# Kernel optimization log

Measured on AMD Instinct MI355X. Metric: run time of the kernel, lower is better.

The kernel has to match this reference:

```python
import jax, jax.numpy as jnp
import numpy as np
from jax.scipy.special import logsumexp

B, T, V, E, H, L = 64, 256, 50000, 256, 256, 9


def setup_inputs() -> dict:
    key = jax.random.key(0)
    ks = jax.random.split(key, 10)
    lengths = jax.random.randint(ks[0], (B,), T // 2, T + 1)
    pm = jnp.arange(T)[None, :] < lengths[:, None]  # valid-token mask, padding at tail
    inp = jnp.where(pm, jax.random.randint(ks[1], (B, T), 1, V), 0).astype(jnp.int32)
    tags = jnp.where(pm, jax.random.randint(ks[2], (B, T), 0, L), 0).astype(jnp.int32)
    s = 0.05
    emb = jax.random.normal(ks[3], (V, E)) * s
    Wf = jax.random.normal(ks[4], (E, 4 * H)) * s
    Uf = jax.random.normal(ks[5], (H, 4 * H)) * s
    bf = jnp.zeros((4 * H,))
    Wb = jax.random.normal(ks[6], (E, 4 * H)) * s
    Ub = jax.random.normal(ks[7], (H, 4 * H)) * s
    bb = jnp.zeros((4 * H,))
    Wd = jax.random.normal(ks[8], (2 * H, L)) * s
    bd = jnp.zeros((L,))
    trans = jax.random.uniform(ks[9], (L, L))
    return dict(inp=inp, tags=tags, emb=emb, Wf=Wf, Uf=Uf, bf=bf,
                Wb=Wb, Ub=Ub, bb=bb, Wd=Wd, bd=bd, trans=trans)


def _lstm(x, mask, W, U, b):
    """Keras-style LSTM with masking (state + output carried through masked steps).
    x: [B,T,E], mask: [B,T] bool -> [B,T,H]."""
    h0 = jnp.zeros((x.shape[0], H), x.dtype)
    c0 = h0

    def step(carry, xm):
        h, c = carry
        xt, mt = xm
        z = xt @ W + h @ U + b  # [B,4H], gate order i,f,g,o (Keras)
        i, f, g, o = jnp.split(z, 4, axis=-1)
        c_new = jax.nn.sigmoid(f) * c + jax.nn.sigmoid(i) * jnp.tanh(g)
        h_new = jax.nn.sigmoid(o) * jnp.tanh(c_new)
        m = mt[:, None]
        h = jnp.where(m, h_new, h)
        c = jnp.where(m, c_new, c)
        return (h, c), h

    _, hs = jax.lax.scan(step, (h0, c0), (x.transpose(1, 0, 2), mask.T))
    return hs.transpose(1, 0, 2)


def _crf_log_likelihood(pot, tags, seq_lens, trans):
    """tfa.text.crf_log_likelihood: sequence_score - log_norm. pot: [B,T,L]."""
    Bv, Tv, Lv = pot.shape
    tmask = (jnp.arange(Tv)[None, :] < seq_lens[:, None]).astype(pot.dtype)
    unary = jnp.sum(jnp.take_along_axis(pot, tags[..., None], axis=-1)[..., 0] * tmask, axis=1)
    pmask = (jnp.arange(Tv - 1)[None, :] < (seq_lens - 1)[:, None]).astype(pot.dtype)
    binary = jnp.sum(trans[tags[:, :-1], tags[:, 1:]] * pmask, axis=1)

    # forward algorithm; alpha frozen once t >= seq_len (tfa uses dynamic_rnn semantics)
    def step(carry, pot_t):
        alpha, t = carry
        new = pot_t + logsumexp(alpha[:, :, None] + trans[None], axis=1)  # [B,L]
        alpha = jnp.where((t < seq_lens)[:, None], new, alpha)
        return (alpha, t + 1), None

    (alpha, _), _ = jax.lax.scan(step, (pot[:, 0, :], jnp.int32(1)),
                                 pot[:, 1:].transpose(1, 0, 2))
    log_norm = logsumexp(alpha, axis=-1)
    return unary + binary - log_norm


def reference(inp, tags, emb, Wf, Uf, bf, Wb, Ub, bb, Wd, bd, trans):
    mask = inp != 0
    seq_lens = jnp.sum(mask.astype(jnp.int32), axis=-1)
    x = jnp.take(emb, inp, axis=0)  # [B,T,E]; dropout is identity (inference)
    hf = _lstm(x, mask, Wf, Uf, bf)
    hb = _lstm(x[:, ::-1], mask[:, ::-1], Wb, Ub, bb)[:, ::-1]
    pot = jnp.concatenate([hf, hb], axis=-1) @ Wd + bd  # [B,T,L]
    ll = _crf_log_likelihood(pot, tags, seq_lens, trans)
    loss = -jnp.mean(ll / seq_lens.astype(pot.dtype))
    return pot, seq_lens, loss
```

## Files before the change

### kernel.cpp

```cpp
#include <hip/hip_runtime.h>

#define B_ 64
#define T_ 256
#define E_ 256
#define H_ 256
#define G4 1024
#define L_ 9

typedef __attribute__((ext_vector_type(8))) short bf16x8;
typedef __attribute__((ext_vector_type(4))) float f32x4;
typedef __attribute__((ext_vector_type(4))) unsigned uint4v;
typedef _Float16 half2v __attribute__((ext_vector_type(2)));

__device__ __forceinline__ ushort f2bf(float x){
  unsigned u = __float_as_uint(x);
  unsigned r = (u + 0x7FFFu + ((u >> 16) & 1u)) >> 16;
  return (ushort)r;
}
__device__ __forceinline__ float bf2f(unsigned u16v){
  return __uint_as_float(u16v << 16);
}
__device__ __forceinline__ float fsig(float x){
  return __builtin_amdgcn_rcpf(1.f + __expf(-x));
}
__device__ __forceinline__ float ftanh(float x){
  return 1.f - 2.f * __builtin_amdgcn_rcpf(__expf(2.f * x) + 1.f);
}
__device__ __forceinline__ int sdot4(unsigned a, unsigned b, int c){
#if __has_builtin(__builtin_amdgcn_sdot4)
  return __builtin_amdgcn_sdot4((int)a, (int)b, c, false);
#else
  int r = c;
  #pragma unroll
  for (int j = 0; j < 4; j++){
    int av = (int)(signed char)((a >> (8 * j)) & 0xFF);
    int bv = (int)(signed char)((b >> (8 * j)) & 0xFF);
    r += av * bv;
  }
  return r;
#endif
}

__global__ void k_prep(const int* __restrict__ inp, const float* __restrict__ emb,
                       const float* __restrict__ Wf, const float* __restrict__ Wb,
                       const float* __restrict__ Uf, const float* __restrict__ Ub,
                       ushort* __restrict__ WT, unsigned* __restrict__ Uq,
                       float* __restrict__ su, ushort* __restrict__ X,
                       int* __restrict__ lens, float* __restrict__ out_len){
  int bid = blockIdx.x, tid = threadIdx.x;
  if (bid < 2048){
    int idx = bid * 256 + tid;
    int dir = idx >> 18; int rem = idx & 262143;
    int n = rem >> 8, k = rem & 255;
    const float* W = dir ? Wb : Wf;
    WT[idx] = f2bf(W[k * G4 + n]);
  } else if (bid < 4096){
    int idx = bid - 2048;
    int dir = idx >> 10, cc = idx & 1023;
    int u = cc & 255, g = cc >> 8;
    const float* U = dir ? Ub : Uf;
    float v = U[tid * G4 + cc];
    __shared__ float red[4];
    __shared__ float ssu;
    __shared__ char qb[256];
    float a = fabsf(v);
    #pragma unroll
    for (int off = 32; off; off >>= 1) a = fmaxf(a, __shfl_xor(a, off));
    int lane = tid & 63, w = tid >> 6;
    if (lane == 0) red[w] = a;
    __syncthreads();
    if (tid == 0){
      float m = fmaxf(fmaxf(red[0], red[1]), fmaxf(red[2], red[3]));
      float s = fmaxf(m, 1e-20f) * (1.f / 127.f);
      ssu = s;
      su[idx] = s;
    }
    __syncthreads();
    float s = ssu;
    int q = __float2int_rn(v / s);
    q = max(-127, min(127, q));
    qb[tid] = (char)q;
    __syncthreads();
    if (tid < 64){
      int khalf = tid >> 5, kk = tid & 31;
      Uq[dir * 65536 + u * 256 + khalf * 128 + g * 32 + kk] =
          *(const unsigned*)&qb[tid * 4];
    }
  } else if (bid < 6144){
    int idx = (bid - 4096) * 256 + tid;
    int m = idx >> 5, koff = (idx & 31) * 8;
    int tok = inp[m];
    const float* src = emb + (size_t)tok * E_ + koff;
    float4 a = *(const float4*)src;
    float4 b = *(const float4*)(src + 4);
    uint4 o;
    o.x = (unsigned)f2bf(a.x) | ((unsigned)f2bf(a.y) << 16);
    o.y = (unsigned)f2bf(a.z) | ((unsigned)f2bf(a.w) << 16);
    o.z = (unsigned)f2bf(b.x) | ((unsigned)f2bf(b.y) << 16);
    o.w = (unsigned)f2bf(b.z) | ((unsigned)f2bf(b.w) << 16);
    *(uint4*)(X + m * E_ + koff) = o;
  } else {
    int w = tid >> 6, lane = tid & 63;
    int b = (bid - 6144) * 4 + w;
    int c = 0;
    for (int t = lane; t < T_; t += 64) c += (inp[b * T_ + t] != 0);
    for (int off = 32; off; off >>= 1) c += __shfl_xor(c, off);
    if (lane == 0){ lens[b] = c; out_len[b] = (float)c; }
  }
}

__global__ __launch_bounds__(256) void k_gemm(const ushort* __restrict__ X,
        const ushort* __restrict__ WT, const float* __restrict__ bf_,
        const float* __restrict__ bb_, ushort* __restrict__ Zpf, ushort* __restrict__ Zpb){
  int zi = blockIdx.z;
  const ushort* wt = WT + zi * 262144;
  const float* bias = zi ? bb_ : bf_;
  ushort* Zp = zi ? Zpb : Zpf;
  int m0 = blockIdx.x * 128, n0 = blockIdx.y * 128;
  __shared__ ushort As[128][40];
  __shared__ ushort Bs[128][40];
  int tid = threadIdx.x;
  int sr = tid >> 1, sk = (tid & 1) * 16;
  const ushort* xg = X + (m0 + sr) * E_ + sk;
  const ushort* wg = wt + (n0 + sr) * E_ + sk;
  f32x4 acc[4][4] = {};
  int lane = tid & 63, wv = tid >> 6;
  int wr = wv >> 1, wc = wv & 1;
  int lrow = lane & 15, kf = (lane >> 4) * 8;
  for (int k0 = 0; k0 < E_; k0 += 32){
    uint4 a0 = *(const uint4*)(xg + k0);
    uint4 a1 = *(const uint4*)(xg + k0 + 8);
    uint4 b0 = *(const uint4*)(wg + k0);
    uint4 b1 = *(const uint4*)(wg + k0 + 8);
    *(uint4*)&As[sr][sk]     = a0;  *(uint4*)&As[sr][sk + 8] = a1;
    *(uint4*)&Bs[sr][sk]     = b0;  *(uint4*)&Bs[sr][sk + 8] = b1;
    __syncthreads();
    bf16x8 af[4], bfr[4];
    #pragma unroll
    for (int i = 0; i < 4; i++) af[i]  = *(const bf16x8*)&As[wr * 64 + i * 16 + lrow][kf];
    #pragma unroll
    for (int i = 0; i < 4; i++) bfr[i] = *(const bf16x8*)&Bs[wc * 64 + i * 16 + lrow][kf];
    #pragma unroll
    for (int i = 0; i < 4; i++)
      #pragma unroll
      for (int j = 0; j < 4; j++)
        acc[i][j] = __builtin_amdgcn_mfma_f32_16x16x32_bf16(af[i], bfr[j], acc[i][j], 0, 0, 0);
    __syncthreads();
  }
  int crow = (lane >> 4) * 4;
  #pragma unroll
  for (int j = 0; j < 4; j++){
    int col = n0 + wc * 64 + j * 16 + lrow;
    float bv = bias[col];
    int gg = col >> 8, jj = col & 255;
    #pragma unroll
    for (int i = 0; i < 4; i++){
      int rbase = m0 + wr * 64 + i * 16 + crow;
      #pragma unroll
      for (int r = 0; r < 4; r++)
        Zp[((size_t)(rbase + r) * 256 + jj) * 4 + gg] = f2bf(acc[i][j][r] + bv);
    }
  }
}

__global__ __launch_bounds__(512, 1) void k_recur11(
    const ushort* __restrict__ Zpf, const ushort* __restrict__ Zpb,
    const unsigned* __restrict__ Uq, const float* __restrict__ su,
    const int* __restrict__ lens, ushort* __restrict__ hf16, ushort* __restrict__ hb16){
  int bid = blockIdx.x;
  int dir = bid >> 6, b = bid & 63;
  const uint2* Zp = (const uint2*)(dir ? Zpb : Zpf);
  ushort* H = dir ? hb16 : hf16;
  int tid = threadIdx.x;
  int u = tid >> 1, khalf = tid & 1;
  float sc0 = su[dir * 1024 +        u] * (1.f / 127.f);
  float sc1 = su[dir * 1024 + 256 +  u] * (1.f / 127.f);
  float sc2 = su[dir * 1024 + 512 +  u] * (1.f / 127.f);
  float sc3 = su[dir * 1024 + 768 +  u] * (1.f / 127.f);
  int alen = lens[b];

  uint4v uq[4][8];
  {
    const unsigned* p = Uq + dir * 65536 + u * 256 + khalf * 128;
    #pragma unroll
    for (int g = 0; g < 4; g++)
      #pragma unroll
      for (int i = 0; i < 8; i++)
        asm volatile("global_load_dwordx4 %0, %1, off"
                     : "=v"(uq[g][i]) : "v"(p + g * 32 + i * 4));
    asm volatile("s_waitcnt vmcnt(0)" ::: "memory");
    __builtin_amdgcn_sched_barrier(0);
  }

  __shared__ unsigned hq[2][64];
  if (tid < 128) ((unsigned*)hq)[tid] = 0u;
  __syncthreads();

  float c_st = 0.f, h_st = 0.f;
  int t0 = dir ? 255 : 0;
  uint2 zw = Zp[(size_t)(b * 256 + t0) * 256 + u];

  for (int s_ = 0; s_ < 256; ++s_){
    int t = dir ? (255 - s_) : s_;
    int tn = dir ? (t - 1) : (t + 1);
    int cur = s_ & 1, nxt = cur ^ 1;
    uint2 zw_n = uint2{0u, 0u};
    if (s_ < 255) zw_n = Zp[(size_t)(b * 256 + tn) * 256 + u];
    int a0 = 0, a1 = 0, a2 = 0, a3 = 0;
    const uint4* hp = (const uint4*)&hq[cur][khalf * 32];
    #pragma unroll
    for (int i = 0; i < 8; i++){
      uint4 hv = hp[i];
      a0 = sdot4(uq[0][i][0], hv.x, a0);  a0 = sdot4(uq[0][i][1], hv.y, a0);
      a0 = sdot4(uq[0][i][2], hv.z, a0);  a0 = sdot4(uq[0][i][3], hv.w, a0);
      a1 = sdot4(uq[1][i][0], hv.x, a1);  a1 = sdot4(uq[1][i][1], hv.y, a1);
      a1 = sdot4(uq[1][i][2], hv.z, a1);  a1 = sdot4(uq[1][i][3], hv.w, a1);
      a2 = sdot4(uq[2][i][0], hv.x, a2);  a2 = sdot4(uq[2][i][1], hv.y, a2);
      a2 = sdot4(uq[2][i][2], hv.z, a2);  a2 = sdot4(uq[2][i][3], hv.w, a2);
      a3 = sdot4(uq[3][i][0], hv.x, a3);  a3 = sdot4(uq[3][i][1], hv.y, a3);
      a3 = sdot4(uq[3][i][2], hv.z, a3);  a3 = sdot4(uq[3][i][3], hv.w, a3);
    }
    a0 += __shfl_xor(a0, 1);
    a1 += __shfl_xor(a1, 1);
    a2 += __shfl_xor(a2, 1);
    a3 += __shfl_xor(a3, 1);
    float zi = bf2f(zw.x & 0xffffu) + (float)a0 * sc0;
    float zf = bf2f(zw.x >> 16)     + (float)a1 * sc1;
    float zg = bf2f(zw.y & 0xffffu) + (float)a2 * sc2;
    float zo = bf2f(zw.y >> 16)     + (float)a3 * sc3;
    if (t < alen){
      c_st = fsig(zf) * c_st + fsig(zi) * ftanh(zg);
      h_st = fsig(zo) * ftanh(c_st);
    }
    if (khalf == 0){
      int ri = __float2int_rn(h_st * 127.f);
      ((char*)hq[nxt])[u] = (char)ri;
      H[(size_t)(b * 256 + t) * H_ + u] = f2bf(h_st);
    }
    __syncthreads();
    zw = zw_n;
  }
}

__global__ __launch_bounds__(256) void k_pot(const ushort* __restrict__ hf16,
        const ushort* __restrict__ hb16, const float* __restrict__ Wd,
        const float* __restrict__ bd, float* __restrict__ out, int* __restrict__ cnt){
  if (blockIdx.x == 0 && threadIdx.x == 0) *cnt = 0;
  int lane = threadIdx.x & 63, wid = threadIdx.x >> 6;
  int m = blockIdx.x * 4 + wid;
  uint2 ua = *(const uint2*)&hf16[(size_t)m * H_ + lane * 4];
  uint2 ub = *(const uint2*)&hb16[(size_t)m * H_ + lane * 4];
  float av[4] = {bf2f(ua.x & 0xFFFFu), bf2f(ua.x >> 16), bf2f(ua.y & 0xFFFFu), bf2f(ua.y >> 16)};
  float bv[4] = {bf2f(ub.x & 0xFFFFu), bf2f(ub.x >> 16), bf2f(ub.y & 0xFFFFu), bf2f(ub.y >> 16)};
  float acc[9];
  #pragma unroll
  for (int l = 0; l < 9; l++) acc[l] = 0.f;
  #pragma unroll
  for (int i = 0; i < 4; i++){
    int r = lane * 4 + i;
    #pragma unroll
    for (int l = 0; l < 9; l++)
      acc[l] += av[i] * Wd[r * 9 + l] + bv[i] * Wd[(H_ + r) * 9 + l];
  }
  #pragma unroll
  for (int off = 32; off; off >>= 1)
    #pragma unroll
    for (int l = 0; l < 9; l++) acc[l] += __shfl_xor(acc[l], off);
  if (lane == 0){
    #pragma unroll
    for (int l = 0; l < 9; l++) out[(size_t)m * 9 + l] = acc[l] + bd[l];
  }
}

__global__ void k_post(const float* __restrict__ out, const int* __restrict__ tags,
                       const float* __restrict__ trans, const int* __restrict__ lens,
                       float* __restrict__ lln, int* cnt, float* __restrict__ loss_out){
  int b = blockIdx.x, lane = threadIdx.x;
  int len = lens[b];
  const float* pot = out + (size_t)b * T_ * 9;
  float up = 0.f, bp = 0.f;
  for (int t = lane; t < T_; t += 64){
    int tg = tags[b * T_ + t];
    if (t < len) up += pot[t * 9 + tg];
    if (t + 1 < len){
      int tg2 = tags[b * T_ + t + 1];
      bp += trans[tg * 9 + tg2];
    }
  }
  for (int off = 32; off; off >>= 1){ up += __shfl_xor(up, off); bp += __shfl_xor(bp, off); }
  float alpha = 0.f;
  if (lane < 9){
    float tr[9];
    #pragma unroll
    for (int i = 0; i < 9; i++) tr[i] = trans[i * 9 + lane];
    alpha = pot[lane];
    for (int t = 1; t < T_; ++t){
      float v[9];
      #pragma unroll
      for (int i = 0; i < 9; i++) v[i] = __shfl(alpha, i) + tr[i];
      float mx = v[0];
      #pragma unroll
      for (int i = 1; i < 9; i++) mx = fmaxf(mx, v[i]);
      float sum = 0.f;
      #pragma unroll
      for (int i = 0; i < 9; i++) sum += __expf(v[i] - mx);
      float an = pot[t * 9 + lane] + mx + __logf(sum);
      if (t < len) alpha = an;
    }
  }
  float mx2 = -3.4e38f;
  for (int i = 0; i < 9; i++){ float a = __shfl(alpha, i); mx2 = fmaxf(mx2, a); }
  float s2 = 0.f;
  for (int i = 0; i < 9; i++){ float a = __shfl(alpha, i); s2 += __expf(a - mx2); }
  float lse = mx2 + __logf(s2);
  __shared__ int lastf;
  if (lane == 0){
    __hip_atomic_store(&lln[b], (up + bp - lse) / (float)len,
                       __ATOMIC_RELAXED, __HIP_MEMORY_SCOPE_AGENT);
    int old = __hip_atomic_fetch_add(cnt, 1, __ATOMIC_ACQ_REL, __HIP_MEMORY_SCOPE_AGENT);
    lastf = (old == 63);
  }
  __syncthreads();
  if (lastf){
    float v = __hip_atomic_load(&lln[lane], __ATOMIC_RELAXED, __HIP_MEMORY_SCOPE_AGENT);
    for (int off = 32; off; off >>= 1) v += __shfl_xor(v, off);
    if (lane == 0) loss_out[0] = -v * (1.f / 64.f);
  }
}

extern "C" void kernel_launch(void* const* d_in, const int* in_sizes, int n_in,
                              void* d_out, int out_size, void* d_ws, size_t ws_size,
                              hipStream_t stream) {
  (void)in_sizes; (void)n_in; (void)out_size; (void)ws_size;
  const int*   inp   = (const int*)  d_in[0];
  const int*   tags  = (const int*)  d_in[1];
  const float* emb   = (const float*)d_in[2];
  const float* Wf    = (const float*)d_in[3];
  const float* Uf    = (const float*)d_in[4];
  const float* bfv   = (const float*)d_in[5];
  const float* Wb    = (const float*)d_in[6];
  const float* Ub    = (const float*)d_in[7];
  const float* bbv   = (const float*)d_in[8];
  const float* Wd    = (const float*)d_in[9];
  const float* bd    = (const float*)d_in[10];
  const float* trans = (const float*)d_in[11];
  float* out = (float*)d_out;

  char* ws = (char*)d_ws;
  unsigned* Uq   = (unsigned*)(ws);
  float*    su   = (float*)   (ws + 524288);
  ushort*   WT16 = (ushort*)  (ws + 1048576);
  ushort*   Xbf  = (ushort*)  (ws + 2097152);
  int*      cnt  = (int*)     (ws + 2097152);
  ushort*   Zpf  = (ushort*)  (ws + 10485760);
  ushort*   Zpb  = (ushort*)  (ws + 44040192);
  ushort*   hf16 = (ushort*)  (ws + 77594624);
  ushort*   hb16 = (ushort*)  (ws + 85983232);
  int*      lens = (int*)     (ws + 94371840);
  float*    lln  = (float*)   (ws + 94372096);

  k_prep<<<6160, 256, 0, stream>>>(inp, emb, Wf, Wb, Uf, Ub, WT16, Uq, su, Xbf,
                                   lens, out + 147456);
  k_gemm<<<dim3(128, 8, 2), 256, 0, stream>>>(Xbf, WT16, bfv, bbv, Zpf, Zpb);
  k_recur11<<<128, 512, 0, stream>>>(Zpf, Zpb, Uq, su, lens, hf16, hb16);
  k_pot<<<4096, 256, 0, stream>>>(hf16, hb16, Wd, bd, out, cnt);
  k_post<<<64, 64, 0, stream>>>(out, tags, trans, lens, lln, cnt, out + 147520);
}
```

Measured before the change: 410.8 us.

## Stage gate preactivations and hidden outputs in LDS in 8-step chunks

The recurrent kernel now prefetches the input-projection gate values for the next 8 timesteps into registers and then into a double-buffered LDS tile, instead of issuing one global load per step. Hidden outputs are collected in LDS and written back as coalesced 32-bit words one chunk later, replacing per-step 16-bit scattered stores. The aim is to take global memory latency off the serial per-step critical path. In exchange it adds LDS usage, extra register staging, and an additional barrier per chunk. Launch bounds now request 2 blocks per CU, which may constrain register allocation for the large register-resident weight array.

```diff
diff --git a/kernel.cpp b/kernel.cpp
--- a/kernel.cpp
+++ b/kernel.cpp
@@ -163,14 +163,14 @@
   }
 }
 
-__global__ __launch_bounds__(512, 1) void k_recur11(
+__global__ __launch_bounds__(512, 2) void k_recur12(
     const ushort* __restrict__ Zpf, const ushort* __restrict__ Zpb,
     const unsigned* __restrict__ Uq, const float* __restrict__ su,
     const int* __restrict__ lens, ushort* __restrict__ hf16, ushort* __restrict__ hb16){
   int bid = blockIdx.x;
   int dir = bid >> 6, b = bid & 63;
   const uint2* Zp = (const uint2*)(dir ? Zpb : Zpf);
-  ushort* H = dir ? hb16 : hf16;
+  unsigned* Hw = (unsigned*)(dir ? hb16 : hf16);
   int tid = threadIdx.x;
   int u = tid >> 1, khalf = tid & 1;
   float sc0 = su[dir * 1024 +        u] * (1.f / 127.f);
@@ -193,52 +193,101 @@
   }
 
   __shared__ unsigned hq[2][64];
+  __shared__ uint2    zbuf[2][8][256];
+  __shared__ ushort   hbufL[2][8][256];
+
+  uint2 zstage[4];
+  #pragma unroll
+  for (int j = 0; j < 4; j++){
+    int e = j * 512 + tid, tt = e >> 8, uu = e & 255;
+    int t = dir ? (255 - tt) : tt;
+    zstage[j] = Zp[(size_t)(b * 256 + t) * 256 + uu];
+  }
   if (tid < 128) ((unsigned*)hq)[tid] = 0u;
+  #pragma unroll
+  for (int j = 0; j < 4; j++){
+    int e = j * 512 + tid;
+    zbuf[0][e >> 8][e & 255] = zstage[j];
+  }
   __syncthreads();
 
   float c_st = 0.f, h_st = 0.f;
-  int t0 = dir ? 255 : 0;
-  uint2 zw = Zp[(size_t)(b * 256 + t0) * 256 + u];
-
-  for (int s_ = 0; s_ < 256; ++s_){
-    int t = dir ? (255 - s_) : s_;
-    int tn = dir ? (t - 1) : (t + 1);
-    int cur = s_ & 1, nxt = cur ^ 1;
-    uint2 zw_n = uint2{0u, 0u};
-    if (s_ < 255) zw_n = Zp[(size_t)(b * 256 + tn) * 256 + u];
-    int a0 = 0, a1 = 0, a2 = 0, a3 = 0;
-    const uint4* hp = (const uint4*)&hq[cur][khalf * 32];
-    #pragma unroll
-    for (int i = 0; i < 8; i++){
-      uint4 hv = hp[i];
-      a0 = sdot4(uq[0][i][0], hv.x, a0);  a0 = sdot4(uq[0][i][1], hv.y, a0);
-      a0 = sdot4(uq[0][i][2], hv.z, a0);  a0 = sdot4(uq[0][i][3], hv.w, a0);
-      a1 = sdot4(uq[1][i][0], hv.x, a1);  a1 = sdot4(uq[1][i][1], hv.y, a1);
-      a1 = sdot4(uq[1][i][2], hv.z, a1);  a1 = sdot4(uq[1][i][3], hv.w, a1);
-      a2 = sdot4(uq[2][i][0], hv.x, a2);  a2 = sdot4(uq[2][i][1], hv.y, a2);
-      a2 = sdot4(uq[2][i][2], hv.z, a2);  a2 = sdot4(uq[2][i][3], hv.w, a2);
-      a3 = sdot4(uq[3][i][0], hv.x, a3);  a3 = sdot4(uq[3][i][1], hv.y, a3);
-      a3 = sdot4(uq[3][i][2], hv.z, a3);  a3 = sdot4(uq[3][i][3], hv.w, a3);
-    }
-    a0 += __shfl_xor(a0, 1);
-    a1 += __shfl_xor(a1, 1);
-    a2 += __shfl_xor(a2, 1);
-    a3 += __shfl_xor(a3, 1);
-    float zi = bf2f(zw.x & 0xffffu) + (float)a0 * sc0;
-    float zf = bf2f(zw.x >> 16)     + (float)a1 * sc1;
-    float zg = bf2f(zw.y & 0xffffu) + (float)a2 * sc2;
-    float zo = bf2f(zw.y >> 16)     + (float)a3 * sc3;
-    if (t < alen){
-      c_st = fsig(zf) * c_st + fsig(zi) * ftanh(zg);
-      h_st = fsig(zo) * ftanh(c_st);
-    }
-    if (khalf == 0){
-      int ri = __float2int_rn(h_st * 127.f);
-      ((char*)hq[nxt])[u] = (char)ri;
-      H[(size_t)(b * 256 + t) * H_ + u] = f2bf(h_st);
-    }
-    __syncthreads();
-    zw = zw_n;
+
+  for (int c = 0; c < 32; ++c){
+    int cb = c & 1;
+    if (c < 31){
+      #pragma unroll
+      for (int j = 0; j < 4; j++){
+        int e = j * 512 + tid, tt = e >> 8, uu = e & 255;
+        int s2 = (c + 1) * 8 + tt;
+        int t = dir ? (255 - s2) : s2;
+        zstage[j] = Zp[(size_t)(b * 256 + t) * 256 + uu];
+      }
+    }
+    if (c > 0){
+      #pragma unroll
+      for (int j = 0; j < 2; j++){
+        int e = j * 512 + tid, tt = e >> 7, p = e & 127;
+        int s2 = (c - 1) * 8 + tt;
+        int t = dir ? (255 - s2) : s2;
+        unsigned wv = ((unsigned*)hbufL[cb ^ 1])[tt * 128 + p];
+        Hw[(size_t)(b * 256 + t) * 128 + p] = wv;
+      }
+    }
+    #pragma unroll
+    for (int tt = 0; tt < 8; ++tt){
+      int s_ = c * 8 + tt;
+      int t = dir ? (255 - s_) : s_;
+      int cur = s_ & 1, nxt = cur ^ 1;
+      uint2 zw = zbuf[cb][tt][u];
+      int a0 = 0, a1 = 0, a2 = 0, a3 = 0;
+      const uint4* hp = (const uint4*)&hq[cur][khalf * 32];
+      #pragma unroll
+      for (int i = 0; i < 8; i++){
+        uint4 hv = hp[i];
+        a0 = sdot4(uq[0][i][0], hv.x, a0);  a0 = sdot4(uq[0][i][1], hv.y, a0);
+        a0 = sdot4(uq[0][i][2], hv.z, a0);  a0 = sdot4(uq[0][i][3], hv.w, a0);
+        a1 = sdot4(uq[1][i][0], hv.x, a1);  a1 = sdot4(uq[1][i][1], hv.y, a1);
+        a1 = sdot4(uq[1][i][2], hv.z, a1);  a1 = sdot4(uq[1][i][3], hv.w, a1);
+        a2 = sdot4(uq[2][i][0], hv.x, a2);  a2 = sdot4(uq[2][i][1], hv.y, a2);
+        a2 = sdot4(uq[2][i][2], hv.z, a2);  a2 = sdot4(uq[2][i][3], hv.w, a2);
+        a3 = sdot4(uq[3][i][0], hv.x, a3);  a3 = sdot4(uq[3][i][1], hv.y, a3);
+        a3 = sdot4(uq[3][i][2], hv.z, a3);  a3 = sdot4(uq[3][i][3], hv.w, a3);
+      }
+      a0 += __shfl_xor(a0, 1);
+      a1 += __shfl_xor(a1, 1);
+      a2 += __shfl_xor(a2, 1);
+      a3 += __shfl_xor(a3, 1);
+      float zi = bf2f(zw.x & 0xffffu) + (float)a0 * sc0;
+      float zf = bf2f(zw.x >> 16)     + (float)a1 * sc1;
+      float zg = bf2f(zw.y & 0xffffu) + (float)a2 * sc2;
+      float zo = bf2f(zw.y >> 16)     + (float)a3 * sc3;
+      if (t < alen){
+        c_st = fsig(zf) * c_st + fsig(zi) * ftanh(zg);
+        h_st = fsig(zo) * ftanh(c_st);
+      }
+      if (khalf == 0){
+        int ri = __float2int_rn(h_st * 127.f);
+        ((char*)hq[nxt])[u] = (char)ri;
+        hbufL[cb][tt][u] = f2bf(h_st);
+      }
+      __syncthreads();
+    }
+    if (c < 31){
+      #pragma unroll
+      for (int j = 0; j < 4; j++){
+        int e = j * 512 + tid;
+        zbuf[cb ^ 1][e >> 8][e & 255] = zstage[j];
+      }
+    }
+    __syncthreads();
+  }
+  #pragma unroll
+  for (int j = 0; j < 2; j++){
+    int e = j * 512 + tid, tt = e >> 7, p = e & 127;
+    int s2 = 248 + tt;
+    int t = dir ? (255 - s2) : s2;
+    Hw[(size_t)(b * 256 + t) * 128 + p] = ((unsigned*)hbufL[1])[tt * 128 + p];
   }
 }
 
@@ -362,7 +411,7 @@
   k_prep<<<6160, 256, 0, stream>>>(inp, emb, Wf, Wb, Uf, Ub, WT16, Uq, su, Xbf,
                                    lens, out + 147456);
   k_gemm<<<dim3(128, 8, 2), 256, 0, stream>>>(Xbf, WT16, bfv, bbv, Zpf, Zpb);
-  k_recur11<<<128, 512, 0, stream>>>(Zpf, Zpb, Uq, su, lens, hf16, hb16);
+  k_recur12<<<128, 512, 0, stream>>>(Zpf, Zpb, Uq, su, lens, hf16, hb16);
   k_pot<<<4096, 256, 0, stream>>>(hf16, hb16, Wd, bd, out, cnt);
   k_post<<<64, 64, 0, stream>>>(out, tags, trans, lens, lln, cnt, out + 147520);
 }
```

After: 411.7 us. Within noise of the previous version (+0.2%).

## Permute gate columns in weight prep, coalesce Z stores, batch LDS h loads

Applied to the files above, without the earlier changes.

The input-weight transpose now permutes gate columns so the GEMM writes each row of Zp contiguously (row*1024+col) rather than scattering strided gate-interleaved stores. U quantization is restructured from 2048 one-column blocks into 32 blocks of 64 columns, with per-column max reduction in shared memory and vectorized uint4 stores. In the recurrence the eight LDS reads of h are hoisted ahead of the dot-product chain behind a sched_barrier, and launch bounds are changed to allow two blocks per CU, which may cost registers held by the quantized U.

```diff
diff --git a/kernel.cpp b/kernel.cpp
--- a/kernel.cpp
+++ b/kernel.cpp
@@ -51,43 +51,66 @@
   if (bid < 2048){
     int idx = bid * 256 + tid;
     int dir = idx >> 18; int rem = idx & 262143;
-    int n = rem >> 8, k = rem & 255;
+    int np = rem >> 8, k = rem & 255;
+    int c = ((np & 3) << 8) | (np >> 2);
     const float* W = dir ? Wb : Wf;
-    WT[idx] = f2bf(W[k * G4 + n]);
-  } else if (bid < 4096){
+    WT[idx] = f2bf(W[k * G4 + c]);
+  } else if (bid < 2080){
     int idx = bid - 2048;
-    int dir = idx >> 10, cc = idx & 1023;
-    int u = cc & 255, g = cc >> 8;
+    int dir = idx >> 4, blk = idx & 15;
+    int c0 = blk * 64;
+    int g = blk >> 2, u0 = (blk & 3) * 64;
     const float* U = dir ? Ub : Uf;
-    float v = U[tid * G4 + cc];
-    __shared__ float red[4];
-    __shared__ float ssu;
-    __shared__ char qb[256];
-    float a = fabsf(v);
-    #pragma unroll
-    for (int off = 32; off; off >>= 1) a = fmaxf(a, __shfl_xor(a, off));
-    int lane = tid & 63, w = tid >> 6;
-    if (lane == 0) red[w] = a;
-    __syncthreads();
-    if (tid == 0){
-      float m = fmaxf(fmaxf(red[0], red[1]), fmaxf(red[2], red[3]));
-      float s = fmaxf(m, 1e-20f) * (1.f / 127.f);
-      ssu = s;
-      su[idx] = s;
-    }
-    __syncthreads();
-    float s = ssu;
-    int q = __float2int_rn(v / s);
-    q = max(-127, min(127, q));
-    qb[tid] = (char)q;
+    int cp = tid & 63, ph = tid >> 6;
+    __shared__ float redA[4][64];
+    __shared__ float rs[64];
+    __shared__ unsigned qbuf[64][64];
+    float am = 0.f;
+    for (int kk = 0; kk < 64; ++kk){
+      float v = U[(size_t)(kk * 4 + ph) * G4 + c0 + cp];
+      am = fmaxf(am, fabsf(v));
+    }
+    redA[ph][cp] = am;
     __syncthreads();
     if (tid < 64){
-      int khalf = tid >> 5, kk = tid & 31;
-      Uq[dir * 65536 + u * 256 + khalf * 128 + g * 32 + kk] =
-          *(const unsigned*)&qb[tid * 4];
-    }
-  } else if (bid < 6144){
-    int idx = (bid - 4096) * 256 + tid;
+      float m = fmaxf(fmaxf(redA[0][tid], redA[1][tid]),
+                      fmaxf(redA[2][tid], redA[3][tid]));
+      float mm = fmaxf(m, 1e-20f);
+      rs[tid] = 127.f / mm;
+      su[dir * 1024 + c0 + tid] = mm * (1.f / 127.f);
+    }
+    __syncthreads();
+    float rsv = rs[cp];
+    for (int w = 0; w < 16; ++w){
+      int kq = ph * 16 + w;
+      unsigned word = 0;
+      #pragma unroll
+      for (int j = 0; j < 4; ++j){
+        float v = U[(size_t)(kq * 4 + j) * G4 + c0 + cp];
+        int q = __float2int_rn(v * rsv);
+        q = max(-127, min(127, q));
+        word |= ((unsigned)(q & 0xFF)) << (8 * j);
+      }
+      qbuf[kq][cp] = word;
+    }
+    __syncthreads();
+    {
+      int uu = tid >> 2, part = tid & 3;
+      int kh = part >> 1, hs = part & 1;
+      unsigned* dst = Uq + dir * 65536 + (u0 + uu) * 256 + kh * 128 + g * 32 + hs * 16;
+      #pragma unroll
+      for (int w4 = 0; w4 < 4; ++w4){
+        int kb = kh * 32 + hs * 16 + w4 * 4;
+        uint4 val;
+        val.x = qbuf[kb + 0][uu];
+        val.y = qbuf[kb + 1][uu];
+        val.z = qbuf[kb + 2][uu];
+        val.w = qbuf[kb + 3][uu];
+        *(uint4*)(dst + w4 * 4) = val;
+      }
+    }
+  } else if (bid < 4128){
+    int idx = (bid - 2080) * 256 + tid;
     int m = idx >> 5, koff = (idx & 31) * 8;
     int tok = inp[m];
     const float* src = emb + (size_t)tok * E_ + koff;
@@ -101,7 +124,7 @@
     *(uint4*)(X + m * E_ + koff) = o;
   } else {
     int w = tid >> 6, lane = tid & 63;
-    int b = (bid - 6144) * 4 + w;
+    int b = (bid - 4128) * 4 + w;
     int c = 0;
     for (int t = lane; t < T_; t += 64) c += (inp[b * T_ + t] != 0);
     for (int off = 32; off; off >>= 1) c += __shfl_xor(c, off);
@@ -151,19 +174,18 @@
   #pragma unroll
   for (int j = 0; j < 4; j++){
     int col = n0 + wc * 64 + j * 16 + lrow;
-    float bv = bias[col];
-    int gg = col >> 8, jj = col & 255;
+    float bv = bias[((col & 3) << 8) | (col >> 2)];
     #pragma unroll
     for (int i = 0; i < 4; i++){
       int rbase = m0 + wr * 64 + i * 16 + crow;
       #pragma unroll
       for (int r = 0; r < 4; r++)
-        Zp[((size_t)(rbase + r) * 256 + jj) * 4 + gg] = f2bf(acc[i][j][r] + bv);
-    }
-  }
-}
-
-__global__ __launch_bounds__(512, 1) void k_recur11(
+        Zp[(size_t)(rbase + r) * 1024 + col] = f2bf(acc[i][j][r] + bv);
+    }
+  }
+}
+
+__global__ __launch_bounds__(512, 2) void k_recur13(
     const ushort* __restrict__ Zpf, const ushort* __restrict__ Zpb,
     const unsigned* __restrict__ Uq, const float* __restrict__ su,
     const int* __restrict__ lens, ushort* __restrict__ hf16, ushort* __restrict__ hb16){
@@ -206,19 +228,23 @@
     int cur = s_ & 1, nxt = cur ^ 1;
     uint2 zw_n = uint2{0u, 0u};
     if (s_ < 255) zw_n = Zp[(size_t)(b * 256 + tn) * 256 + u];
+    const uint4* hp = (const uint4*)&hq[cur][khalf * 32];
+    uint4 hv[8];
+    #pragma unroll
+    for (int i = 0; i < 8; i++) hv[i] = hp[i];
+    __builtin_amdgcn_sched_barrier(0);
     int a0 = 0, a1 = 0, a2 = 0, a3 = 0;
-    const uint4* hp = (const uint4*)&hq[cur][khalf * 32];
     #pragma unroll
     for (int i = 0; i < 8; i++){
-      uint4 hv = hp[i];
-      a0 = sdot4(uq[0][i][0], hv.x, a0);  a0 = sdot4(uq[0][i][1], hv.y, a0);
-      a0 = sdot4(uq[0][i][2], hv.z, a0);  a0 = sdot4(uq[0][i][3], hv.w, a0);
-      a1 = sdot4(uq[1][i][0], hv.x, a1);  a1 = sdot4(uq[1][i][1], hv.y, a1);
-      a1 = sdot4(uq[1][i][2], hv.z, a1);  a1 = sdot4(uq[1][i][3], hv.w, a1);
-      a2 = sdot4(uq[2][i][0], hv.x, a2);  a2 = sdot4(uq[2][i][1], hv.y, a2);
-      a2 = sdot4(uq[2][i][2], hv.z, a2);  a2 = sdot4(uq[2][i][3], hv.w, a2);
-      a3 = sdot4(uq[3][i][0], hv.x, a3);  a3 = sdot4(uq[3][i][1], hv.y, a3);
-      a3 = sdot4(uq[3][i][2], hv.z, a3);  a3 = sdot4(uq[3][i][3], hv.w, a3);
+      uint4 hvv = hv[i];
+      a0 = sdot4(uq[0][i][0], hvv.x, a0);  a0 = sdot4(uq[0][i][1], hvv.y, a0);
+      a0 = sdot4(uq[0][i][2], hvv.z, a0);  a0 = sdot4(uq[0][i][3], hvv.w, a0);
+      a1 = sdot4(uq[1][i][0], hvv.x, a1);  a1 = sdot4(uq[1][i][1], hvv.y, a1);
+      a1 = sdot4(uq[1][i][2], hvv.z, a1);  a1 = sdot4(uq[1][i][3], hvv.w, a1);
+      a2 = sdot4(uq[2][i][0], hvv.x, a2);  a2 = sdot4(uq[2][i][1], hvv.y, a2);
+      a2 = sdot4(uq[2][i][2], hvv.z, a2);  a2 = sdot4(uq[2][i][3], hvv.w, a2);
+      a3 = sdot4(uq[3][i][0], hvv.x, a3);  a3 = sdot4(uq[3][i][1], hvv.y, a3);
+      a3 = sdot4(uq[3][i][2], hvv.z, a3);  a3 = sdot4(uq[3][i][3], hvv.w, a3);
     }
     a0 += __shfl_xor(a0, 1);
     a1 += __shfl_xor(a1, 1);
@@ -359,10 +385,10 @@
   int*      lens = (int*)     (ws + 94371840);
   float*    lln  = (float*)   (ws + 94372096);
 
-  k_prep<<<6160, 256, 0, stream>>>(inp, emb, Wf, Wb, Uf, Ub, WT16, Uq, su, Xbf,
+  k_prep<<<4144, 256, 0, stream>>>(inp, emb, Wf, Wb, Uf, Ub, WT16, Uq, su, Xbf,
                                    lens, out + 147456);
   k_gemm<<<dim3(128, 8, 2), 256, 0, stream>>>(Xbf, WT16, bfv, bbv, Zpf, Zpb);
-  k_recur11<<<128, 512, 0, stream>>>(Zpf, Zpb, Uq, su, lens, hf16, hb16);
+  k_recur13<<<128, 512, 0, stream>>>(Zpf, Zpb, Uq, su, lens, hf16, hb16);
   k_pot<<<4096, 256, 0, stream>>>(hf16, hb16, Wd, bd, out, cnt);
   k_post<<<64, 64, 0, stream>>>(out, tags, trans, lens, lln, cnt, out + 147520);
 }
```

After: 394.0 us. 1.04x faster.
